# Kernel optimization log

Hardware: AMD Instinct MI355X
Metric: run time of the kernel (lower is better)

The kernel has to match this reference:

```python
import jax, jax.numpy as jnp
import numpy as np

N_NODES = 200000
N_EDGES = 640000
D_NODE = 128   # NO_NODE_FEATURES_TWO
D_EDGE = 32    # NO_EDGE_FEATURES_TWO
HIDDEN = 128   # HIDDEN_NODE_TWO


def setup_inputs() -> dict:
    key = jax.random.key(0)
    ks = jax.random.split(key, 8)
    x = jax.random.normal(ks[0], (N_NODES, D_NODE), dtype=jnp.float32)
    edge_index = jax.random.randint(ks[1], (2, N_EDGES), 0, N_NODES, dtype=jnp.int64)
    edge_attr = jax.random.normal(ks[2], (N_EDGES, D_EDGE), dtype=jnp.float32)
    u = jax.random.normal(ks[3], (64, D_NODE), dtype=jnp.float32)
    batch = jax.random.randint(ks[4], (N_NODES,), 0, 64, dtype=jnp.int64)
    # Xavier-uniform linear weights (stored as [in, out]); bias filled with 0.01 as in init_weights
    def xavier(k, fan_in, fan_out):
        limit = float(np.sqrt(6.0 / (fan_in + fan_out)))
        return jax.random.uniform(k, (fan_in, fan_out), jnp.float32, -limit, limit)
    W1 = xavier(ks[5], D_EDGE + D_NODE, HIDDEN)          # [160, 128]
    b1 = jnp.full((HIDDEN,), 0.01, dtype=jnp.float32)
    W2 = xavier(ks[6], HIDDEN + D_NODE, D_NODE)          # [256, 128]
    b2 = jnp.full((D_NODE,), 0.01, dtype=jnp.float32)
    return {"x": x, "edge_index": edge_index, "edge_attr": edge_attr,
            "u": u, "batch": batch, "W1": W1, "b1": b1, "W2": W2, "b2": b2}


def reference(x, edge_index, edge_attr, u, batch, W1, b1, W2, b2):
    row, col = edge_index[0], edge_index[1]
    # gather source-node features, concat with edge features: [E, 160]
    msg = jnp.concatenate([x[row], edge_attr], axis=1)
    msg = msg @ W1 + b1                                   # [E, hidden]
    # scatter_add by destination node
    agg = jax.ops.segment_sum(msg, col, num_segments=x.shape[0])  # [N, hidden]
    out = jnp.concatenate([x, agg], axis=1)               # [N, 256]
    return out @ W2 + b2                                  # [N, 128]
```

## Files before the change

kernel.cpp:

```cpp
#include <hip/hip_runtime.h>
#include <hip/hip_bf16.h>

#define N_NODES 200000
#define N_EDGES 640000
#define D_NODE 128
#define D_EDGE 32
#define HIDDEN 128
#define KTOT 288

using bf16x8  = __attribute__((ext_vector_type(8))) short;
using f32x4   = __attribute__((ext_vector_type(4))) float;
using short4v = __attribute__((ext_vector_type(4))) short;

__device__ __forceinline__ short f2b(float f) {
  return __builtin_bit_cast(short, __float2bfloat16(f));
}
__device__ __forceinline__ float b2f(short s) {
  unsigned u = ((unsigned)(unsigned short)s) << 16;
  return __builtin_bit_cast(float, u);
}

__device__ __forceinline__ void prep_body(const float* __restrict__ x,
                                          short* __restrict__ xb,
                                          int pblk, int tid) {
  const int i = pblk * 256 + tid;
  const int node = i >> 4;
  const int oct  = (i & 15) << 3;
  const float4 v0 = *(const float4*)&x[(size_t)node * D_NODE + oct];
  const float4 v1 = *(const float4*)&x[(size_t)node * D_NODE + oct + 4];
  bf16x8 o = { f2b(v0.x), f2b(v0.y), f2b(v0.z), f2b(v0.w),
               f2b(v1.x), f2b(v1.y), f2b(v1.z), f2b(v1.w) };
  *(bf16x8*)&xb[(size_t)node * D_NODE + oct] = o;
}

#define MIX_NB 8750
#define WC_NB  145

__global__ __launch_bounds__(256) void k_histprep(
    const int* __restrict__ ei, int* cnt, int* slot,
    const float* __restrict__ x, short* __restrict__ xb,
    const float* __restrict__ W1, const float* __restrict__ b1,
    const float* __restrict__ W2, short* __restrict__ WcT,
    float* __restrict__ bc)
{
  const int b = blockIdx.x;
  const int tid = threadIdx.x;
  if (b < MIX_NB) {
    const int g = b / 7, r = b % 7;
    if (r < 2) {
      const int e = (g * 2 + r) * 256 + tid;
      slot[e] = atomicAdd(&cnt[ei[N_EDGES + e]], 1);
    } else {
      prep_body(x, xb, g * 5 + (r - 2), tid);
    }
  } else {
    const int t = (b - MIX_NB) * 256 + tid;
    if (t < 288 * 128) {
      const int brow = t >> 7, c = t & 127;
      if (brow < 128) {
        WcT[c * KTOT + brow] = f2b(W2[brow * 128 + c]);
      } else {
        const int i = brow - 128;
        float acc = 0.f;
        #pragma unroll 8
        for (int q = 0; q < 128; ++q)
          acc += W1[i * 128 + q] * W2[(128 + q) * 128 + c];
        WcT[c * KTOT + brow] = f2b(acc);
      }
    } else if (t < 288 * 128 + 128) {
      const int c = t - 288 * 128;
      float acc = 0.f;
      #pragma unroll 8
      for (int q = 0; q < 128; ++q)
        acc += b1[q] * W2[(128 + q) * 128 + c];
      bc[c] = acc;
    }
  }
}

#define SCAN_NB 196

__global__ __launch_bounds__(256) void k_scan_a(const int* __restrict__ cnt,
                                                int* bsum) {
  __shared__ int sh[256];
  const int b = blockIdx.x, t = threadIdx.x;
  const int base = b * 1024 + t * 4;
  int s = 0;
  #pragma unroll
  for (int k = 0; k < 4; ++k) {
    const int idx = base + k;
    s += (idx < N_NODES) ? cnt[idx] : 0;
  }
  sh[t] = s; __syncthreads();
  for (int o = 128; o > 0; o >>= 1) {
    if (t < o) sh[t] += sh[t + o];
    __syncthreads();
  }
  if (t == 0) bsum[b] = sh[0];
}

__global__ __launch_bounds__(256) void k_scan_c2(const int* __restrict__ cnt,
                                                 const int* __restrict__ bsum,
                                                 int* offv) {
  __shared__ int sh[256];
  __shared__ int base_sh;
  const int b = blockIdx.x, t = threadIdx.x;

  sh[t] = (t < SCAN_NB && t < b) ? bsum[t] : 0;
  __syncthreads();
  for (int o = 128; o > 0; o >>= 1) {
    if (t < o) sh[t] += sh[t + o];
    __syncthreads();
  }
  if (t == 0) base_sh = sh[0];
  __syncthreads();

  const int base = b * 1024 + t * 4;
  int v[4], p[4], s = 0;
  #pragma unroll
  for (int k = 0; k < 4; ++k) {
    const int idx = base + k;
    v[k] = (idx < N_NODES) ? cnt[idx] : 0;
    p[k] = s; s += v[k];
  }
  sh[t] = s; __syncthreads();
  const int tot = s;
  for (int o = 1; o < 256; o <<= 1) {
    const int tv = (t >= o) ? sh[t - o] : 0;
    __syncthreads();
    sh[t] += tv;
    __syncthreads();
  }
  const int gb = base_sh + (sh[t] - tot);
  #pragma unroll
  for (int k = 0; k < 4; ++k) {
    const int idx = base + k;
    if (idx < N_NODES) offv[idx] = gb + p[k];
  }
}

__global__ __launch_bounds__(256) void k_placeprep2(
    const int* __restrict__ ei, const int* __restrict__ offv,
    const int* __restrict__ slot, const float* __restrict__ ea,
    int* __restrict__ psrc, short* __restrict__ ea_s,
    const float* __restrict__ x, short* __restrict__ xb)
{
  const int b = blockIdx.x;
  const int tid = threadIdx.x;
  const int g = b / 7, r = b % 7;
  if (r < 2) {
    const int e = (g * 2 + r) * 256 + tid;
    const int j = offv[ei[N_EDGES + e]] + slot[e];
    psrc[j] = ei[e];
    #pragma unroll
    for (int h = 0; h < 4; ++h) {
      const float4 w0 = *(const float4*)&ea[(size_t)e * D_EDGE + h * 8];
      const float4 w1 = *(const float4*)&ea[(size_t)e * D_EDGE + h * 8 + 4];
      bf16x8 o = { f2b(w0.x), f2b(w0.y), f2b(w0.z), f2b(w0.w),
                   f2b(w1.x), f2b(w1.y), f2b(w1.z), f2b(w1.w) };
      *(bf16x8*)&ea_s[(size_t)j * D_EDGE + h * 8] = o;
    }
  } else {
    prep_body(x, xb, 6250 + g * 5 + (r - 2), tid);
  }
}

__global__ __launch_bounds__(256) void k_sagg4(
    const int* __restrict__ offv, const int* __restrict__ cnt,
    const int* __restrict__ psrc, const short* __restrict__ xb,
    const short* __restrict__ ea_s,
    short* __restrict__ Sx, short* __restrict__ Se)
{
  const int gtid = blockIdx.x * 256 + threadIdx.x;
  if (gtid < N_NODES * 16) {
    const int node = gtid >> 4;
    const int oct8 = (gtid & 15) << 3;
    const int s0 = offv[node];
    const int s1 = s0 + cnt[node];
    float a[8] = {};
    int j = s0;
    while (j < s1) {
      const int rem = s1 - j;
      bf16x8 v0, v1, v2, v3;
      v0 = *(const bf16x8*)&xb[(size_t)psrc[j] * D_NODE + oct8];
      if (rem > 1) v1 = *(const bf16x8*)&xb[(size_t)psrc[j + 1] * D_NODE + oct8];
      if (rem > 2) v2 = *(const bf16x8*)&xb[(size_t)psrc[j + 2] * D_NODE + oct8];
      if (rem > 3) v3 = *(const bf16x8*)&xb[(size_t)psrc[j + 3] * D_NODE + oct8];
      #pragma unroll
      for (int k = 0; k < 8; ++k) a[k] += b2f(v0[k]);
      if (rem > 1) {
        #pragma unroll
        for (int k = 0; k < 8; ++k) a[k] += b2f(v1[k]);
      }
      if (rem > 2) {
        #pragma unroll
        for (int k = 0; k < 8; ++k) a[k] += b2f(v2[k]);
      }
      if (rem > 3) {
        #pragma unroll
        for (int k = 0; k < 8; ++k) a[k] += b2f(v3[k]);
      }
      j += 4;
    }
    bf16x8 o;
    #pragma unroll
    for (int k = 0; k < 8; ++k) o[k] = f2b(a[k]);
    *(bf16x8*)&Sx[(size_t)node * D_NODE + oct8] = o;
  } else {
    const int t2 = gtid - N_NODES * 16;
    const int node = t2 >> 2;
    const int q8   = (t2 & 3) << 3;
    const int s0 = offv[node];
    const int s1 = s0 + cnt[node];
    float a[8] = {};
    for (int j = s0; j < s1; ++j) {
      const bf16x8 v = *(const bf16x8*)&ea_s[(size_t)j * D_EDGE + q8];
      #pragma unroll
      for (int k = 0; k < 8; ++k) a[k] += b2f(v[k]);
    }
    bf16x8 o;
    #pragma unroll
    for (int k = 0; k < 8; ++k) o[k] = f2b(a[k]);
    *(bf16x8*)&Se[(size_t)node * D_EDGE + q8] = o;
  }
}

#define LDP 104

__global__ __launch_bounds__(256, 4) void k_out2(
    const short* __restrict__ xb, const short* __restrict__ Sx,
    const short* __restrict__ Se, const short* __restrict__ WcT,
    const float* __restrict__ bc, const float* __restrict__ b2,
    const int* __restrict__ cnt, float* __restrict__ out)
{
  __shared__ short smem[64 * LDP + 128 * LDP];
  short* lA = smem;
  short* lB = smem + 64 * LDP;
  const int tid = threadIdx.x;
  const int n0  = blockIdx.x * 64;

  const int lane = tid & 63;
  const int wid  = tid >> 6;
  const int wm = wid >> 1, wn = wid & 1;
  const int lrow = lane & 15;
  const int lk   = (lane >> 4) << 3;

  f32x4 acc[2][4] = {};

  #pragma unroll
  for (int p = 0; p < 3; ++p) {
    for (int i = tid; i < 1536; i += 256) {
      const int n = i / 12, ck = (i % 12) << 3;
      *(bf16x8*)&lB[n * LDP + ck] = *(const bf16x8*)&WcT[n * KTOT + p * 96 + ck];
    }
    for (int i = tid; i < 768; i += 256) {
      const int m = i / 12, ck = (i % 12) << 3;
      const int k = p * 96 + ck;
      const int node = n0 + m;
      const short* src;
      if (k < 128)      src = &xb[(size_t)node * D_NODE + k];
      else if (k < 256) src = &Sx[(size_t)node * D_NODE + (k - 128)];
      else              src = &Se[(size_t)node * D_EDGE + (k - 256)];
      *(bf16x8*)&lA[m * LDP + ck] = *(const bf16x8*)src;
    }
    __syncthreads();
    #pragma unroll
    for (int kt = 0; kt < 3; ++kt) {
      const int ks = kt * 32 + lk;
      bf16x8 af[2], bfr[4];
      #pragma unroll
      for (int i = 0; i < 2; ++i)
        af[i]  = *(const bf16x8*)&lA[(wm * 32 + i * 16 + lrow) * LDP + ks];
      #pragma unroll
      for (int j = 0; j < 4; ++j)
        bfr[j] = *(const bf16x8*)&lB[(wn * 64 + j * 16 + lrow) * LDP + ks];
      #pragma unroll
      for (int i = 0; i < 2; ++i)
        #pragma unroll
        for (int j = 0; j < 4; ++j)
          acc[i][j] = __builtin_amdgcn_mfma_f32_16x16x32_bf16(af[i], bfr[j], acc[i][j], 0, 0, 0);
    }
    __syncthreads();
  }

  float* lf = (float*)smem;
  const int rb = wm * 32 + ((lane >> 4) << 2);
  const int cb = wn * 64 + lrow;
  float bcv[4], b2v[4];
  #pragma unroll
  for (int j = 0; j < 4; ++j) {
    bcv[j] = bc[cb + j * 16];
    b2v[j] = b2[cb + j * 16];
  }
  #pragma unroll
  for (int i = 0; i < 2; ++i) {
    #pragma unroll
    for (int r = 0; r < 4; ++r) {
      const int row = rb + i * 16 + r;
      const float cf = (float)cnt[n0 + row];
      #pragma unroll
      for (int j = 0; j < 4; ++j)
        lf[row * 128 + cb + j * 16] = acc[i][j][r] + cf * bcv[j] + b2v[j];
    }
  }
  __syncthreads();
  #pragma unroll
  for (int u = 0; u < 8; ++u) {
    const int idx = tid + u * 256;
    const int row = idx >> 5, f4 = (idx & 31) << 2;
    *(float4*)&out[(size_t)(n0 + row) * HIDDEN + f4] = *(const float4*)&lf[row * 128 + f4];
  }
}

extern "C" void kernel_launch(void* const* d_in, const int* in_sizes, int n_in,
                              void* d_out, int out_size, void* d_ws, size_t ws_size,
                              hipStream_t stream) {
  const float* x  = (const float*)d_in[0];
  const int*   ei = (const int*)d_in[1];
  const float* ea = (const float*)d_in[2];
  const float* W1 = (const float*)d_in[5];
  const float* b1 = (const float*)d_in[6];
  const float* W2 = (const float*)d_in[7];
  const float* b2 = (const float*)d_in[8];
  float* out = (float*)d_out;

  const size_t XB_B   = (size_t)N_NODES * D_NODE * 2;
  const size_t SX_B   = (size_t)N_NODES * D_NODE * 2;
  const size_t SE_B   = (size_t)N_NODES * D_EDGE * 2;
  const size_t WCT_B  = 128 * KTOT * 2;
  const size_t BC_B   = 512;
  const size_t CNT_B  = (size_t)N_NODES * 4;
  const size_t SLOT_B = (size_t)N_EDGES * 4;
  const size_t PSRC_B = (size_t)N_EDGES * 4;
  const size_t EAS_B  = (size_t)N_EDGES * D_EDGE * 2;

  const size_t o_xb   = 0;
  const size_t o_sx   = o_xb + XB_B;
  const size_t o_se   = o_sx + SX_B;
  const size_t o_wct  = o_se + SE_B;
  const size_t o_bc   = o_wct + WCT_B;
  const size_t o_cnt  = o_bc + BC_B;
  const size_t o_off  = o_cnt + CNT_B;
  const size_t o_slot = o_off + CNT_B;
  const size_t o_psrc = o_slot + SLOT_B;
  const size_t o_eas  = o_psrc + PSRC_B;
  const size_t o_bsum = o_eas + EAS_B;

  short* xb   = (short*)((char*)d_ws + o_xb);
  short* Sx   = (short*)((char*)d_ws + o_sx);
  short* Se   = (short*)((char*)d_ws + o_se);
  short* WcT  = (short*)((char*)d_ws + o_wct);
  float* bc   = (float*)((char*)d_ws + o_bc);
  int*   cnt  = (int*)((char*)d_ws + o_cnt);
  int*   offv = (int*)((char*)d_ws + o_off);
  int*   slot = (int*)((char*)d_ws + o_slot);
  int*   psrc = (int*)((char*)d_ws + o_psrc);
  short* ea_s = (short*)((char*)d_ws + o_eas);
  int*   bsum = (int*)((char*)d_ws + o_bsum);

  hipMemsetAsync(cnt, 0, CNT_B, stream);
  k_histprep<<<MIX_NB + WC_NB, 256, 0, stream>>>(ei, cnt, slot, x, xb,
                                                 W1, b1, W2, WcT, bc);

  k_scan_a <<<SCAN_NB, 256, 0, stream>>>(cnt, bsum);
  k_scan_c2<<<SCAN_NB, 256, 0, stream>>>(cnt, bsum, offv);

  k_placeprep2<<<MIX_NB, 256, 0, stream>>>(ei, offv, slot, ea,
                                           psrc, ea_s, x, xb);

  k_sagg4<<<(N_NODES * 20) / 256, 256, 0, stream>>>(offv, cnt, psrc, xb, ea_s, Sx, Se);
  k_out2 <<<N_NODES / 64, 256, 0, stream>>>(xb, Sx, Se, WcT, bc, b2, cnt, out);
}
```

Measured before the change: 207.4 us.

## Fuse edge-attr aggregation into output GEMM loader and use atomic cursors for CSR placement

Removes the Se intermediate by summing the sorted edge attributes per node directly while staging the A tile in the output GEMM kernel. The aggregation kernel now handles only node-feature gathers. The per-edge slot array is replaced by atomic increments on a copy of the offsets during placement, so the histogram pass no longer writes slots. This saves global traffic and a buffer, but the GEMM loader now carries a variable-length loop, and the second atomic pass changes the order of edges within each segment.

After: 234.9 us. 13.3% more time.

```diff
diff --git a/kernel.cpp b/kernel.cpp
--- a/kernel.cpp
+++ b/kernel.cpp
@@ -37,7 +37,7 @@
 #define WC_NB  145
 
 __global__ __launch_bounds__(256) void k_histprep(
-    const int* __restrict__ ei, int* cnt, int* slot,
+    const int* __restrict__ ei, int* cnt,
     const float* __restrict__ x, short* __restrict__ xb,
     const float* __restrict__ W1, const float* __restrict__ b1,
     const float* __restrict__ W2, short* __restrict__ WcT,
@@ -49,7 +49,7 @@
     const int g = b / 7, r = b % 7;
     if (r < 2) {
       const int e = (g * 2 + r) * 256 + tid;
-      slot[e] = atomicAdd(&cnt[ei[N_EDGES + e]], 1);
+      atomicAdd(&cnt[ei[N_EDGES + e]], 1);
     } else {
       prep_body(x, xb, g * 5 + (r - 2), tid);
     }
@@ -101,7 +101,7 @@
 
 __global__ __launch_bounds__(256) void k_scan_c2(const int* __restrict__ cnt,
                                                  const int* __restrict__ bsum,
-                                                 int* offv) {
+                                                 int* offv, int* offcur) {
   __shared__ int sh[256];
   __shared__ int base_sh;
   const int b = blockIdx.x, t = threadIdx.x;
@@ -135,13 +135,17 @@
   #pragma unroll
   for (int k = 0; k < 4; ++k) {
     const int idx = base + k;
-    if (idx < N_NODES) offv[idx] = gb + p[k];
+    if (idx < N_NODES) {
+      const int o = gb + p[k];
+      offv[idx]   = o;
+      offcur[idx] = o;
+    }
   }
 }
 
 __global__ __launch_bounds__(256) void k_placeprep2(
-    const int* __restrict__ ei, const int* __restrict__ offv,
-    const int* __restrict__ slot, const float* __restrict__ ea,
+    const int* __restrict__ ei, int* __restrict__ offcur,
+    const float* __restrict__ ea,
     int* __restrict__ psrc, short* __restrict__ ea_s,
     const float* __restrict__ x, short* __restrict__ xb)
 {
@@ -150,7 +154,8 @@
   const int g = b / 7, r = b % 7;
   if (r < 2) {
     const int e = (g * 2 + r) * 256 + tid;
-    const int j = offv[ei[N_EDGES + e]] + slot[e];
+    const int dst = ei[N_EDGES + e];
+    const int j = atomicAdd(&offcur[dst], 1);
     psrc[j] = ei[e];
     #pragma unroll
     for (int h = 0; h < 4; ++h) {
@@ -168,68 +173,50 @@
 __global__ __launch_bounds__(256) void k_sagg4(
     const int* __restrict__ offv, const int* __restrict__ cnt,
     const int* __restrict__ psrc, const short* __restrict__ xb,
-    const short* __restrict__ ea_s,
-    short* __restrict__ Sx, short* __restrict__ Se)
+    short* __restrict__ Sx)
 {
   const int gtid = blockIdx.x * 256 + threadIdx.x;
-  if (gtid < N_NODES * 16) {
-    const int node = gtid >> 4;
-    const int oct8 = (gtid & 15) << 3;
-    const int s0 = offv[node];
-    const int s1 = s0 + cnt[node];
-    float a[8] = {};
-    int j = s0;
-    while (j < s1) {
-      const int rem = s1 - j;
-      bf16x8 v0, v1, v2, v3;
-      v0 = *(const bf16x8*)&xb[(size_t)psrc[j] * D_NODE + oct8];
-      if (rem > 1) v1 = *(const bf16x8*)&xb[(size_t)psrc[j + 1] * D_NODE + oct8];
-      if (rem > 2) v2 = *(const bf16x8*)&xb[(size_t)psrc[j + 2] * D_NODE + oct8];
-      if (rem > 3) v3 = *(const bf16x8*)&xb[(size_t)psrc[j + 3] * D_NODE + oct8];
-      #pragma unroll
-      for (int k = 0; k < 8; ++k) a[k] += b2f(v0[k]);
-      if (rem > 1) {
-        #pragma unroll
-        for (int k = 0; k < 8; ++k) a[k] += b2f(v1[k]);
-      }
-      if (rem > 2) {
-        #pragma unroll
-        for (int k = 0; k < 8; ++k) a[k] += b2f(v2[k]);
-      }
-      if (rem > 3) {
-        #pragma unroll
-        for (int k = 0; k < 8; ++k) a[k] += b2f(v3[k]);
-      }
-      j += 4;
-    }
-    bf16x8 o;
+  const int node = gtid >> 4;
+  const int oct8 = (gtid & 15) << 3;
+  const int s0 = offv[node];
+  const int s1 = s0 + cnt[node];
+  float a[8] = {};
+  int j = s0;
+  while (j < s1) {
+    const int rem = s1 - j;
+    bf16x8 v0, v1, v2, v3;
+    v0 = *(const bf16x8*)&xb[(size_t)psrc[j] * D_NODE + oct8];
+    if (rem > 1) v1 = *(const bf16x8*)&xb[(size_t)psrc[j + 1] * D_NODE + oct8];
+    if (rem > 2) v2 = *(const bf16x8*)&xb[(size_t)psrc[j + 2] * D_NODE + oct8];
+    if (rem > 3) v3 = *(const bf16x8*)&xb[(size_t)psrc[j + 3] * D_NODE + oct8];
     #pragma unroll
-    for (int k = 0; k < 8; ++k) o[k] = f2b(a[k]);
-    *(bf16x8*)&Sx[(size_t)node * D_NODE + oct8] = o;
-  } else {
-    const int t2 = gtid - N_NODES * 16;
-    const int node = t2 >> 2;
-    const int q8   = (t2 & 3) << 3;
-    const int s0 = offv[node];
-    const int s1 = s0 + cnt[node];
-    float a[8] = {};
-    for (int j = s0; j < s1; ++j) {
-      const bf16x8 v = *(const bf16x8*)&ea_s[(size_t)j * D_EDGE + q8];
-      #pragma unroll
-      for (int k = 0; k < 8; ++k) a[k] += b2f(v[k]);
-    }
-    bf16x8 o;
-    #pragma unroll
-    for (int k = 0; k < 8; ++k) o[k] = f2b(a[k]);
-    *(bf16x8*)&Se[(size_t)node * D_EDGE + q8] = o;
-  }
+    for (int k = 0; k < 8; ++k) a[k] += b2f(v0[k]);
+    if (rem > 1) {
+      #pragma unroll
+      for (int k = 0; k < 8; ++k) a[k] += b2f(v1[k]);
+    }
+    if (rem > 2) {
+      #pragma unroll
+      for (int k = 0; k < 8; ++k) a[k] += b2f(v2[k]);
+    }
+    if (rem > 3) {
+      #pragma unroll
+      for (int k = 0; k < 8; ++k) a[k] += b2f(v3[k]);
+    }
+    j += 4;
+  }
+  bf16x8 o;
+  #pragma unroll
+  for (int k = 0; k < 8; ++k) o[k] = f2b(a[k]);
+  *(bf16x8*)&Sx[(size_t)node * D_NODE + oct8] = o;
 }
 
 #define LDP 104
 
 __global__ __launch_bounds__(256, 4) void k_out2(
     const short* __restrict__ xb, const short* __restrict__ Sx,
-    const short* __restrict__ Se, const short* __restrict__ WcT,
+    const short* __restrict__ ea_s, const int* __restrict__ offv,
+    const short* __restrict__ WcT,
     const float* __restrict__ bc, const float* __restrict__ b2,
     const int* __restrict__ cnt, float* __restrict__ out)
 {
@@ -257,11 +244,25 @@
       const int m = i / 12, ck = (i % 12) << 3;
       const int k = p * 96 + ck;
       const int node = n0 + m;
-      const short* src;
-      if (k < 128)      src = &xb[(size_t)node * D_NODE + k];
-      else if (k < 256) src = &Sx[(size_t)node * D_NODE + (k - 128)];
-      else              src = &Se[(size_t)node * D_EDGE + (k - 256)];
-      *(bf16x8*)&lA[m * LDP + ck] = *(const bf16x8*)src;
+      if (k < 128) {
+        *(bf16x8*)&lA[m * LDP + ck] = *(const bf16x8*)&xb[(size_t)node * D_NODE + k];
+      } else if (k < 256) {
+        *(bf16x8*)&lA[m * LDP + ck] = *(const bf16x8*)&Sx[(size_t)node * D_NODE + (k - 128)];
+      } else {
+        const int qg = k - 256;
+        const int s0 = offv[node];
+        const int s1 = s0 + cnt[node];
+        float a[8] = {};
+        for (int j = s0; j < s1; ++j) {
+          const bf16x8 v = *(const bf16x8*)&ea_s[(size_t)j * D_EDGE + qg];
+          #pragma unroll
+          for (int kk = 0; kk < 8; ++kk) a[kk] += b2f(v[kk]);
+        }
+        bf16x8 o;
+        #pragma unroll
+        for (int kk = 0; kk < 8; ++kk) o[kk] = f2b(a[kk]);
+        *(bf16x8*)&lA[m * LDP + ck] = o;
+      }
     }
     __syncthreads();
     #pragma unroll
@@ -326,48 +327,43 @@
 
   const size_t XB_B   = (size_t)N_NODES * D_NODE * 2;
   const size_t SX_B   = (size_t)N_NODES * D_NODE * 2;
-  const size_t SE_B   = (size_t)N_NODES * D_EDGE * 2;
   const size_t WCT_B  = 128 * KTOT * 2;
   const size_t BC_B   = 512;
   const size_t CNT_B  = (size_t)N_NODES * 4;
-  const size_t SLOT_B = (size_t)N_EDGES * 4;
   const size_t PSRC_B = (size_t)N_EDGES * 4;
   const size_t EAS_B  = (size_t)N_EDGES * D_EDGE * 2;
 
   const size_t o_xb   = 0;
   const size_t o_sx   = o_xb + XB_B;
-  const size_t o_se   = o_sx + SX_B;
-  const size_t o_wct  = o_se + SE_B;
+  const size_t o_wct  = o_sx + SX_B;
   const size_t o_bc   = o_wct + WCT_B;
   const size_t o_cnt  = o_bc + BC_B;
   const size_t o_off  = o_cnt + CNT_B;
-  const size_t o_slot = o_off + CNT_B;
-  const size_t o_psrc = o_slot + SLOT_B;
+  const size_t o_ofc  = o_off + CNT_B;
+  const size_t o_psrc = o_ofc + CNT_B;
   const size_t o_eas  = o_psrc + PSRC_B;
   const size_t o_bsum = o_eas + EAS_B;
 
-  short* xb   = (short*)((char*)d_ws + o_xb);
-  short* Sx   = (short*)((char*)d_ws + o_sx);
-  short* Se   = (short*)((char*)d_ws + o_se);
-  short* WcT  = (short*)((char*)d_ws + o_wct);
-  float* bc   = (float*)((char*)d_ws + o_bc);
-  int*   cnt  = (int*)((char*)d_ws + o_cnt);
-  int*   offv = (int*)((char*)d_ws + o_off);
-  int*   slot = (int*)((char*)d_ws + o_slot);
-  int*   psrc = (int*)((char*)d_ws + o_psrc);
-  short* ea_s = (short*)((char*)d_ws + o_eas);
-  int*   bsum = (int*)((char*)d_ws + o_bsum);
+  short* xb     = (short*)((char*)d_ws + o_xb);
+  short* Sx     = (short*)((char*)d_ws + o_sx);
+  short* WcT    = (short*)((char*)d_ws + o_wct);
+  float* bc     = (float*)((char*)d_ws + o_bc);
+  int*   cnt    = (int*)((char*)d_ws + o_cnt);
+  int*   offv   = (int*)((char*)d_ws + o_off);
+  int*   offcur = (int*)((char*)d_ws + o_ofc);
+  int*   psrc   = (int*)((char*)d_ws + o_psrc);
+  short* ea_s   = (short*)((char*)d_ws + o_eas);
+  int*   bsum   = (int*)((char*)d_ws + o_bsum);
 
   hipMemsetAsync(cnt, 0, CNT_B, stream);
-  k_histprep<<<MIX_NB + WC_NB, 256, 0, stream>>>(ei, cnt, slot, x, xb,
+  k_histprep<<<MIX_NB + WC_NB, 256, 0, stream>>>(ei, cnt, x, xb,
                                                  W1, b1, W2, WcT, bc);
 
   k_scan_a <<<SCAN_NB, 256, 0, stream>>>(cnt, bsum);
-  k_scan_c2<<<SCAN_NB, 256, 0, stream>>>(cnt, bsum, offv);
-
-  k_placeprep2<<<MIX_NB, 256, 0, stream>>>(ei, offv, slot, ea,
-                                           psrc, ea_s, x, xb);
-
-  k_sagg4<<<(N_NODES * 20) / 256, 256, 0, stream>>>(offv, cnt, psrc, xb, ea_s, Sx, Se);
-  k_out2 <<<N_NODES / 64, 256, 0, stream>>>(xb, Sx, Se, WcT, bc, b2, cnt, out);
-}
+  k_scan_c2<<<SCAN_NB, 256, 0, stream>>>(cnt, bsum, offv, offcur);
+
+  k_placeprep2<<<MIX_NB, 256, 0, stream>>>(ei, offcur, ea, psrc, ea_s, x, xb);
+
+  k_sagg4<<<(N_NODES * 16) / 256, 256, 0, stream>>>(offv, cnt, psrc, xb, Sx);
+  k_out2 <<<N_NODES / 64, 256, 0, stream>>>(xb, Sx, ea_s, offv, WcT, bc, b2, cnt, out);
+}
```
